# Performance work log

Measured on AMD Instinct MI355X. Metric: run time of the kernel, lower is better.

The kernel has to match this reference:

```python
import jax, jax.numpy as jnp
import numpy as np

INPUT_DIM = 1024
EMBED_DIM = 1024
NUM_HEADS = 16
HEAD_DIM = EMBED_DIM // NUM_HEADS


def setup_inputs() -> dict:
    key = jax.random.key(0)
    k_x, k_qkv, k_w, k_b = jax.random.split(key, 4)
    B, N = 2, 2048
    x = jax.random.normal(k_x, (B, N, INPUT_DIM), dtype=jnp.float32)
    # nn.Linear weights: stored [out, in]; scale like torch default init
    s1 = 1.0 / np.sqrt(INPUT_DIM)
    s2 = 1.0 / np.sqrt(EMBED_DIM)
    W_qkv = jax.random.uniform(k_qkv, (3 * EMBED_DIM, INPUT_DIM), jnp.float32, -s1, s1)
    W_out = jax.random.uniform(k_w, (EMBED_DIM, EMBED_DIM), jnp.float32, -s2, s2)
    b_out = jax.random.uniform(k_b, (EMBED_DIM,), jnp.float32, -s2, s2)
    return {"x": x, "W_qkv": W_qkv, "W_out": W_out, "b_out": b_out}


def reference(x, W_qkv, W_out, b_out):
    B, N, C = x.shape
    # qkv projection (no bias): [B, N, 3*embed]
    qkv = jnp.einsum('bnc,ec->bne', x, W_qkv)
    q = qkv[:, :, 0:EMBED_DIM].reshape(B, N, NUM_HEADS, HEAD_DIM)
    k = qkv[:, :, EMBED_DIM:2 * EMBED_DIM].reshape(B, N, NUM_HEADS, HEAD_DIM)
    v = qkv[:, :, 2 * EMBED_DIM:3 * EMBED_DIM].reshape(B, N, NUM_HEADS, HEAD_DIM)
    scores = jnp.einsum('bihd,bjhd->bhij', q, k) / jnp.sqrt(jnp.float32(HEAD_DIM))
    attn = jax.nn.softmax(scores, axis=-1)
    out = jnp.einsum('bhij,bjhd->bihd', attn, v).reshape(B, N, EMBED_DIM)
    return jnp.einsum('bne,oe->bno', out, W_out) + b_out
```

## Files before the change

kernel.cpp:

```cpp
#include <hip/hip_runtime.h>
#include <stdint.h>

typedef __attribute__((ext_vector_type(8))) short short8;
typedef __attribute__((ext_vector_type(4))) short bf16x4;
typedef __attribute__((ext_vector_type(4))) float f32x4;

#define MFMA32(a, b, c) __builtin_amdgcn_mfma_f32_16x16x32_bf16((a), (b), (c), 0, 0, 0)

__device__ __forceinline__ uint16_t f32_to_bf16(float f) {
  union { float f; uint32_t u; } v; v.f = f;
  uint32_t u = v.u;
  u += 0x7FFFu + ((u >> 16) & 1u);
  return (uint16_t)(u >> 16);
}
__device__ __forceinline__ uint16_t f32_to_bf16_fast(float f) {
  union { float f; uint32_t u; } v; v.f = f;
  return (uint16_t)((v.u + 0x8000u) >> 16);
}

__device__ __forceinline__ void load_lds16(const uint16_t* g, uint16_t* l) {
  __builtin_amdgcn_global_load_lds(
      (const __attribute__((address_space(1))) uint32_t*)g,
      (__attribute__((address_space(3))) uint32_t*)l, 16, 0, 0);
}

__global__ __launch_bounds__(256) void cvt3_kernel(
    const float* __restrict__ x, const float* __restrict__ w1,
    const float* __restrict__ w2, uint16_t* __restrict__ xb,
    uint16_t* __restrict__ w1b, uint16_t* __restrict__ w2b) {
  const int i = blockIdx.x * 256 + threadIdx.x;
  const float4* src;
  ushort4* dst;
  int off;
  if (i < 1048576) { src = (const float4*)x;  dst = (ushort4*)xb;  off = i; }
  else if (i < 1835008) { src = (const float4*)w1; dst = (ushort4*)w1b; off = i - 1048576; }
  else { src = (const float4*)w2; dst = (ushort4*)w2b; off = i - 1835008; }
  const float4 v = src[off];
  ushort4 o;
  o.x = f32_to_bf16(v.x);
  o.y = f32_to_bf16(v.y);
  o.z = f32_to_bf16(v.z);
  o.w = f32_to_bf16(v.w);
  dst[off] = o;
}

__global__ __launch_bounds__(256) void gemm_qkv_kernel(
    const uint16_t* __restrict__ A, const uint16_t* __restrict__ Bt,
    uint16_t* __restrict__ Qh, uint16_t* __restrict__ Kh, uint16_t* __restrict__ Vh) {
  __shared__ __align__(16) uint16_t As[128 * 64];
  __shared__ __align__(16) uint16_t Bs[64 * 64];
  const int tid = threadIdx.x;
  const int wave = tid >> 6;
  const int lane = tid & 63;
  const int quad = lane >> 4;
  const int l16 = lane & 15;
  const int row0 = blockIdx.x * 128;
  const int col0 = blockIdx.y * 64;
  const int wm = (wave >> 1) * 64;
  const int wn = (wave & 1) * 32;
  const int K = 1024;

  f32x4 acc[4][2];
#pragma unroll
  for (int a = 0; a < 4; ++a)
#pragma unroll
    for (int b = 0; b < 2; ++b) acc[a][b] = (f32x4){0.f, 0.f, 0.f, 0.f};

  const int swz8 = ((lane & 7) ^ ((lane >> 3) & 7)) * 8;
  const uint16_t* gA = A + (size_t)(row0 + wave * 32 + (lane >> 3)) * K + swz8;
  const uint16_t* gB = Bt + (size_t)(col0 + wave * 16 + (lane >> 3)) * K + swz8;

  for (int k0 = 0; k0 < K; k0 += 64) {
#pragma unroll
    for (int s = 0; s < 4; ++s)
      load_lds16(gA + (size_t)s * 8 * K + k0, &As[(wave * 32 + s * 8) * 64]);
#pragma unroll
    for (int s = 0; s < 2; ++s)
      load_lds16(gB + (size_t)s * 8 * K + k0, &Bs[(wave * 16 + s * 8) * 64]);
    __syncthreads();
#pragma unroll
    for (int ks = 0; ks < 2; ++ks) {
      const int cswz = (((ks * 4 + quad) ^ (l16 & 7)) * 8);
      short8 af[4], bf[2];
#pragma unroll
      for (int mt = 0; mt < 4; ++mt)
        af[mt] = *(const short8*)&As[(wm + mt * 16 + l16) * 64 + cswz];
#pragma unroll
      for (int nt = 0; nt < 2; ++nt)
        bf[nt] = *(const short8*)&Bs[(wn + nt * 16 + l16) * 64 + cswz];
#pragma unroll
      for (int mt = 0; mt < 4; ++mt)
#pragma unroll
        for (int nt = 0; nt < 2; ++nt)
          acc[mt][nt] = MFMA32(af[mt], bf[nt], acc[mt][nt]);
    }
    __syncthreads();
  }

#pragma unroll
  for (int mt = 0; mt < 4; ++mt) {
#pragma unroll
    for (int nt = 0; nt < 2; ++nt) {
      const int col = col0 + wn + nt * 16 + l16;
      const int which = col >> 10;
      const int hc = (col & 1023) >> 6;
      const int d = col & 63;
#pragma unroll
      for (int r = 0; r < 4; ++r) {
        const int row = row0 + wm + mt * 16 + quad * 4 + r;
        const float val = acc[mt][nt][r];
        const int b = row >> 11;
        const int nn = row & 2047;
        const size_t hb = (size_t)(b * 16 + hc) * 131072;
        if (which == 0) {
          Qh[hb + (size_t)nn * 64 + d] = f32_to_bf16(val * 0.1803368801111244f);
        } else if (which == 1) {
          const uint16_t bv = f32_to_bf16(val);
          const int jt = nn >> 6, st = (nn >> 4) & 3, j16 = nn & 15;
          const int kc = d >> 5, qd = (d >> 3) & 3, e = d & 7;
          Kh[hb + jt * 4096 + st * 1024 + kc * 512 + (qd * 16 + j16) * 8 + e] = bv;
        } else {
          const uint16_t bv = f32_to_bf16(val);
          const int jt = nn >> 6, jp = nn & 63;
          const int st2 = jp >> 5, j32 = jp & 31;
          const int qv = (j32 >> 2) & 3, e = (j32 >> 4) * 4 + (j32 & 3);
          const int dt = d >> 4, d16 = d & 15;
          Vh[hb + jt * 4096 + (st2 * 4 + dt) * 512 + (qv * 16 + d16) * 8 + e] = bv;
        }
      }
    }
  }
}

__global__ __launch_bounds__(256) void gemm_out_kernel(
    const uint16_t* __restrict__ A, const uint16_t* __restrict__ Bt,
    float* __restrict__ Cf, const float* __restrict__ bias) {
  __shared__ __align__(16) uint16_t As[64 * 64];
  __shared__ __align__(16) uint16_t Bs[64 * 64];
  const int tid = threadIdx.x;
  const int wave = tid >> 6;
  const int lane = tid & 63;
  const int quad = lane >> 4;
  const int l16 = lane & 15;
  const int row0 = blockIdx.x * 64;
  const int col0 = blockIdx.y * 64;
  const int wm = (wave >> 1) * 32;
  const int wn = (wave & 1) * 32;
  const int K = 1024;
  const int N = 1024;

  f32x4 acc[2][2];
#pragma unroll
  for (int a = 0; a < 2; ++a)
#pragma unroll
    for (int b = 0; b < 2; ++b) acc[a][b] = (f32x4){0.f, 0.f, 0.f, 0.f};

  const int swz8 = ((lane & 7) ^ ((lane >> 3) & 7)) * 8;
  const uint16_t* gA = A + (size_t)(row0 + wave * 16 + (lane >> 3)) * K + swz8;
  const uint16_t* gB = Bt + (size_t)(col0 + wave * 16 + (lane >> 3)) * K + swz8;

  for (int k0 = 0; k0 < K; k0 += 64) {
#pragma unroll
    for (int s = 0; s < 2; ++s) {
      load_lds16(gA + (size_t)s * 8 * K + k0, &As[(wave * 16 + s * 8) * 64]);
      load_lds16(gB + (size_t)s * 8 * K + k0, &Bs[(wave * 16 + s * 8) * 64]);
    }
    __syncthreads();
#pragma unroll
    for (int ks = 0; ks < 2; ++ks) {
      const int cswz = (((ks * 4 + quad) ^ (l16 & 7)) * 8);
      short8 af[2], bf[2];
#pragma unroll
      for (int mt = 0; mt < 2; ++mt)
        af[mt] = *(const short8*)&As[(wm + mt * 16 + l16) * 64 + cswz];
#pragma unroll
      for (int nt = 0; nt < 2; ++nt)
        bf[nt] = *(const short8*)&Bs[(wn + nt * 16 + l16) * 64 + cswz];
#pragma unroll
      for (int mt = 0; mt < 2; ++mt)
#pragma unroll
        for (int nt = 0; nt < 2; ++nt)
          acc[mt][nt] = MFMA32(af[mt], bf[nt], acc[mt][nt]);
    }
    __syncthreads();
  }

#pragma unroll
  for (int mt = 0; mt < 2; ++mt) {
#pragma unroll
    for (int nt = 0; nt < 2; ++nt) {
      const int col = col0 + wn + nt * 16 + l16;
#pragma unroll
      for (int r = 0; r < 4; ++r) {
        const int row = row0 + wm + mt * 16 + quad * 4 + r;
        Cf[(size_t)row * N + col] = acc[mt][nt][r] + bias[col];
      }
    }
  }
}

__global__ __launch_bounds__(256, 4) void attn_kernel(
    const uint16_t* __restrict__ Qh, const uint16_t* __restrict__ Kh,
    const uint16_t* __restrict__ Vh, uint16_t* __restrict__ out) {
  __shared__ __align__(16) uint16_t Ks[2][4096];
  __shared__ __align__(16) uint16_t Vs[2][4096];
  const int tid = threadIdx.x;
  const int wave = tid >> 6;
  const int lane = tid & 63;
  const int quad = lane >> 4;
  const int l16 = lane & 15;
  const int bx = blockIdx.x;
  const int xcd = bx & 7;
  const int g = bx >> 3;
  const int it = g & 31;
  const int h = ((g >> 5) & 1) * 8 + xcd;
  const int ib = g >> 6;
  const int i0 = it * 64 + wave * 16;
  const size_t hb = (size_t)(ib * 16 + h) * 131072;

  short8 qf[2];
#pragma unroll
  for (int kc = 0; kc < 2; ++kc)
    qf[kc] = *(const short8*)(Qh + hb + (size_t)(i0 + l16) * 64 + kc * 32 + quad * 8);

  f32x4 o[4], o4;
  o4 = (f32x4){0.f, 0.f, 0.f, 0.f};
#pragma unroll
  for (int t = 0; t < 4; ++t) o[t] = (f32x4){0.f, 0.f, 0.f, 0.f};

  const short8 ones8 = {(short)0x3F80, (short)0x3F80, (short)0x3F80, (short)0x3F80,
                        (short)0x3F80, (short)0x3F80, (short)0x3F80, (short)0x3F80};

  const uint16_t* gK = Kh + hb + wave * 1024 + lane * 8;
  const uint16_t* gV = Vh + hb + wave * 1024 + lane * 8;
  const int so = wave * 1024;

  load_lds16(gK, &Ks[0][so]);
  load_lds16(gK + 512, &Ks[0][so + 512]);
  load_lds16(gV, &Vs[0][so]);
  load_lds16(gV + 512, &Vs[0][so + 512]);
  __syncthreads();

#pragma unroll 2
  for (int t = 0; t < 32; ++t) {
    const int cur = t & 1;
    if (t < 31) {
      const size_t goff = (size_t)(t + 1) * 4096;
      load_lds16(gK + goff, &Ks[cur ^ 1][so]);
      load_lds16(gK + goff + 512, &Ks[cur ^ 1][so + 512]);
      load_lds16(gV + goff, &Vs[cur ^ 1][so]);
      load_lds16(gV + goff + 512, &Vs[cur ^ 1][so + 512]);
    }

    short8 kf[8];
#pragma unroll
    for (int i = 0; i < 8; ++i) kf[i] = *(const short8*)&Ks[cur][i * 512 + lane * 8];

    f32x4 s[4];
    __builtin_amdgcn_s_setprio(1);
#pragma unroll
    for (int st = 0; st < 4; ++st) {
      f32x4 sc = (f32x4){0.f, 0.f, 0.f, 0.f};
      sc = MFMA32(kf[st * 2 + 0], qf[0], sc);
      sc = MFMA32(kf[st * 2 + 1], qf[1], sc);
      s[st] = sc;
    }
    __builtin_amdgcn_s_setprio(0);

    short8 v8[8];
#pragma unroll
    for (int i = 0; i < 8; ++i) v8[i] = *(const short8*)&Vs[cur][i * 512 + lane * 8];

    short8 p8[2];
#pragma unroll
    for (int st2 = 0; st2 < 2; ++st2) {
      short8 p;
#pragma unroll
      for (int hh = 0; hh < 2; ++hh)
#pragma unroll
        for (int r = 0; r < 4; ++r)
          p[hh * 4 + r] =
              (short)f32_to_bf16_fast(__builtin_amdgcn_exp2f(s[st2 * 2 + hh][r]));
      p8[st2] = p;
    }

    __builtin_amdgcn_s_setprio(1);
#pragma unroll
    for (int st2 = 0; st2 < 2; ++st2) {
      o4 = MFMA32(p8[st2], ones8, o4);
#pragma unroll
      for (int dt = 0; dt < 4; ++dt)
        o[dt] = MFMA32(p8[st2], v8[st2 * 4 + dt], o[dt]);
    }
    __builtin_amdgcn_s_setprio(0);

    __syncthreads();
  }

#pragma unroll
  for (int r = 0; r < 4; ++r) {
    const float inv = 1.0f / o4[r];
    const int row = i0 + quad * 4 + r;
    const size_t obase = (size_t)(ib * 2048 + row) * 1024 + h * 64;
#pragma unroll
    for (int tt = 0; tt < 4; ++tt)
      out[obase + tt * 16 + l16] = f32_to_bf16(o[tt][r] * inv);
  }
}

extern "C" void kernel_launch(void* const* d_in, const int* in_sizes, int n_in,
                              void* d_out, int out_size, void* d_ws, size_t ws_size,
                              hipStream_t stream) {
  const float* x = (const float*)d_in[0];
  const float* Wqkv = (const float*)d_in[1];
  const float* Wout = (const float*)d_in[2];
  const float* bout = (const float*)d_in[3];

  uint16_t* xb = (uint16_t*)d_ws;
  uint16_t* wqkvb = xb + (size_t)4096 * 1024;
  uint16_t* woutb = wqkvb + (size_t)3072 * 1024;
  uint16_t* qh = woutb + (size_t)1024 * 1024;
  uint16_t* kh = qh + (size_t)32 * 131072;
  uint16_t* vh = kh + (size_t)32 * 131072;
  uint16_t* attnb = vh + (size_t)32 * 131072;

  cvt3_kernel<<<8192, 256, 0, stream>>>(x, Wqkv, Wout, xb, wqkvb, woutb);

  gemm_qkv_kernel<<<dim3(4096 / 128, 3072 / 64), 256, 0, stream>>>(
      xb, wqkvb, qh, kh, vh);

  attn_kernel<<<1024, 256, 0, stream>>>(qh, kh, vh, attnb);

  gemm_out_kernel<<<dim3(4096 / 64, 1024 / 64), 256, 0, stream>>>(
      attnb, woutb, (float*)d_out, bout);
}
```

Before: 178.4 us.

## Split attention waves into query and key groups with LDS partial-sum reduction

Each wave now handles 32 query rows over half of every 64-key tile, where before it handled 16 query rows over the whole tile. This halves the per-wave K and V LDS fragment reads and reuses each K fragment across two query subtiles. At the end the two key-group halves reduce their numerator and denominator accumulators through LDS, and only half the waves write output. The cost is an extra barrier and reduction step, and more accumulator registers per wave.

```diff
diff --git a/kernel.cpp b/kernel.cpp
--- a/kernel.cpp
+++ b/kernel.cpp
@@ -209,24 +209,32 @@
   const int lane = tid & 63;
   const int quad = lane >> 4;
   const int l16 = lane & 15;
+  const int qg = wave >> 1;
+  const int kg = wave & 1;
   const int bx = blockIdx.x;
   const int xcd = bx & 7;
   const int g = bx >> 3;
   const int it = g & 31;
   const int h = ((g >> 5) & 1) * 8 + xcd;
   const int ib = g >> 6;
-  const int i0 = it * 64 + wave * 16;
+  const int i0 = it * 64 + qg * 32;
   const size_t hb = (size_t)(ib * 16 + h) * 131072;
 
-  short8 qf[2];
-#pragma unroll
-  for (int kc = 0; kc < 2; ++kc)
-    qf[kc] = *(const short8*)(Qh + hb + (size_t)(i0 + l16) * 64 + kc * 32 + quad * 8);
-
-  f32x4 o[4], o4;
-  o4 = (f32x4){0.f, 0.f, 0.f, 0.f};
-#pragma unroll
-  for (int t = 0; t < 4; ++t) o[t] = (f32x4){0.f, 0.f, 0.f, 0.f};
+  short8 qf[2][2];
+#pragma unroll
+  for (int m = 0; m < 2; ++m)
+#pragma unroll
+    for (int kc = 0; kc < 2; ++kc)
+      qf[m][kc] = *(const short8*)(Qh + hb + (size_t)(i0 + m * 16 + l16) * 64 +
+                                   kc * 32 + quad * 8);
+
+  f32x4 o[2][4], o4[2];
+#pragma unroll
+  for (int m = 0; m < 2; ++m) {
+    o4[m] = (f32x4){0.f, 0.f, 0.f, 0.f};
+#pragma unroll
+    for (int t = 0; t < 4; ++t) o[m][t] = (f32x4){0.f, 0.f, 0.f, 0.f};
+  }
 
   const short8 ones8 = {(short)0x3F80, (short)0x3F80, (short)0x3F80, (short)0x3F80,
                         (short)0x3F80, (short)0x3F80, (short)0x3F80, (short)0x3F80};
@@ -252,59 +260,87 @@
       load_lds16(gV + goff + 512, &Vs[cur ^ 1][so + 512]);
     }
 
-    short8 kf[8];
-#pragma unroll
-    for (int i = 0; i < 8; ++i) kf[i] = *(const short8*)&Ks[cur][i * 512 + lane * 8];
-
-    f32x4 s[4];
+    short8 kf[2][2];
+#pragma unroll
+    for (int kt = 0; kt < 2; ++kt)
+#pragma unroll
+      for (int kc = 0; kc < 2; ++kc)
+        kf[kt][kc] =
+            *(const short8*)&Ks[cur][(kg * 2 + kt) * 1024 + kc * 512 + lane * 8];
+
+    f32x4 s[2][2];
     __builtin_amdgcn_s_setprio(1);
 #pragma unroll
-    for (int st = 0; st < 4; ++st) {
-      f32x4 sc = (f32x4){0.f, 0.f, 0.f, 0.f};
-      sc = MFMA32(kf[st * 2 + 0], qf[0], sc);
-      sc = MFMA32(kf[st * 2 + 1], qf[1], sc);
-      s[st] = sc;
-    }
+    for (int kt = 0; kt < 2; ++kt)
+#pragma unroll
+      for (int m = 0; m < 2; ++m) {
+        f32x4 sc = (f32x4){0.f, 0.f, 0.f, 0.f};
+        sc = MFMA32(kf[kt][0], qf[m][0], sc);
+        sc = MFMA32(kf[kt][1], qf[m][1], sc);
+        s[kt][m] = sc;
+      }
     __builtin_amdgcn_s_setprio(0);
 
-    short8 v8[8];
-#pragma unroll
-    for (int i = 0; i < 8; ++i) v8[i] = *(const short8*)&Vs[cur][i * 512 + lane * 8];
+    short8 v8[4];
+#pragma unroll
+    for (int dt = 0; dt < 4; ++dt)
+      v8[dt] = *(const short8*)&Vs[cur][(kg * 4 + dt) * 512 + lane * 8];
 
     short8 p8[2];
 #pragma unroll
-    for (int st2 = 0; st2 < 2; ++st2) {
+    for (int m = 0; m < 2; ++m) {
       short8 p;
 #pragma unroll
-      for (int hh = 0; hh < 2; ++hh)
+      for (int kt = 0; kt < 2; ++kt)
 #pragma unroll
         for (int r = 0; r < 4; ++r)
-          p[hh * 4 + r] =
-              (short)f32_to_bf16_fast(__builtin_amdgcn_exp2f(s[st2 * 2 + hh][r]));
-      p8[st2] = p;
+          p[kt * 4 + r] =
+              (short)f32_to_bf16_fast(__builtin_amdgcn_exp2f(s[kt][m][r]));
+      p8[m] = p;
     }
 
     __builtin_amdgcn_s_setprio(1);
 #pragma unroll
-    for (int st2 = 0; st2 < 2; ++st2) {
-      o4 = MFMA32(p8[st2], ones8, o4);
+    for (int m = 0; m < 2; ++m) {
+      o4[m] = MFMA32(p8[m], ones8, o4[m]);
 #pragma unroll
       for (int dt = 0; dt < 4; ++dt)
-        o[dt] = MFMA32(p8[st2], v8[st2 * 4 + dt], o[dt]);
+        o[m][dt] = MFMA32(p8[m], v8[dt], o[m][dt]);
     }
     __builtin_amdgcn_s_setprio(0);
 
     __syncthreads();
   }
 
-#pragma unroll
-  for (int r = 0; r < 4; ++r) {
-    const float inv = 1.0f / o4[r];
-    const int row = i0 + quad * 4 + r;
-    const size_t obase = (size_t)(ib * 2048 + row) * 1024 + h * 64;
-#pragma unroll
-    for (int tt = 0; tt < 4; ++tt)
-      out[obase + tt * 16 + l16] = f32_to_bf16(o[tt][r] * inv);
+  float* fKs = (float*)&Ks[0][0];
+  float* fVs = (float*)&Vs[0][0];
+  if (kg == 1) {
+#pragma unroll
+    for (int m = 0; m < 2; ++m) {
+      *(f32x4*)&fVs[(qg * 2 + m) * 256 + lane * 4] = o4[m];
+#pragma unroll
+      for (int dt = 0; dt < 4; ++dt)
+        *(f32x4*)&fKs[((qg * 2 + m) * 4 + dt) * 256 + lane * 4] = o[m][dt];
+    }
+  }
+  __syncthreads();
+  if (kg == 0) {
+#pragma unroll
+    for (int m = 0; m < 2; ++m) {
+      const f32x4 l1 = *(const f32x4*)&fVs[(qg * 2 + m) * 256 + lane * 4];
+#pragma unroll
+      for (int dt = 0; dt < 4; ++dt)
+        o[m][dt] += *(const f32x4*)&fKs[((qg * 2 + m) * 4 + dt) * 256 + lane * 4];
+#pragma unroll
+      for (int r = 0; r < 4; ++r) {
+        const float inv = 1.0f / (o4[m][r] + l1[r]);
+        const int row = i0 + m * 16 + quad * 4 + r;
+        const size_t obase = (size_t)(ib * 2048 + row) * 1024 + h * 64;
+#pragma unroll
+        for (int dt = 0; dt < 4; ++dt)
+          out[obase + dt * 16 + l16] = f32_to_bf16(o[m][dt][r] * inv);
+      }
+    }
   }
 }
 
```

Result: no change. 177.1 us (-0.7%).
